# Kernel optimization log

Measured on AMD Instinct MI355X. Metric: run time of the kernel, lower is better.

The kernel has to match this reference:

```python
import jax, jax.numpy as jnp
import numpy as np

HIDDEN = 2048
NUM_HEADS = 16
NUM_KV_HEADS = 4
HEAD_DIM = 128
ROPE_BASE = 10000.0


def apply_rope(x):
    # x: [B, H, S, D]; standard half-split RoPE
    B, H, S, D = x.shape
    half = D // 2
    inv_freq = 1.0 / (ROPE_BASE ** (jnp.arange(half, dtype=jnp.float32) / half))
    ang = jnp.arange(S, dtype=jnp.float32)[:, None] * inv_freq[None, :]  # [S, half]
    cos = jnp.cos(ang).astype(x.dtype)
    sin = jnp.sin(ang).astype(x.dtype)
    x1, x2 = x[..., :half], x[..., half:]
    return jnp.concatenate([x1 * cos - x2 * sin, x1 * sin + x2 * cos], axis=-1)


def setup_inputs() -> dict:
    key = jax.random.key(0)
    ks = jax.random.split(key, 6)
    B, S = 2, 2048
    sd = 1.0 / np.sqrt(HIDDEN)
    x = jax.random.normal(ks[0], (B, S, HIDDEN), dtype=jnp.float32)
    wq = jax.random.normal(ks[1], (NUM_HEADS * HEAD_DIM, HIDDEN), dtype=jnp.float32) * sd
    wk = jax.random.normal(ks[2], (NUM_KV_HEADS * HEAD_DIM, HIDDEN), dtype=jnp.float32) * sd
    wv = jax.random.normal(ks[3], (NUM_KV_HEADS * HEAD_DIM, HIDDEN), dtype=jnp.float32) * sd
    wo = jax.random.normal(ks[4], (HIDDEN, NUM_HEADS * HEAD_DIM), dtype=jnp.float32) * sd
    key_weights = jnp.ones((NUM_HEADS,), dtype=jnp.float32)
    return {"x": x, "wq": wq, "wk": wk, "wv": wv, "wo": wo, "key_weights": key_weights}


def reference(x, wq, wk, wv, wo, key_weights):
    B, S, _ = x.shape
    g = NUM_HEADS // NUM_KV_HEADS
    scale = HEAD_DIM ** -0.5
    # projections -> [B, H, S, D]
    q = (x @ wq.T).reshape(B, S, NUM_HEADS, HEAD_DIM).transpose(0, 2, 1, 3)
    k = (x @ wk.T).reshape(B, S, NUM_KV_HEADS, HEAD_DIM).transpose(0, 2, 1, 3)
    v = (x @ wv.T).reshape(B, S, NUM_KV_HEADS, HEAD_DIM).transpose(0, 2, 1, 3)
    q = apply_rope(q)
    k = apply_rope(k)
    # GQA expansion (repeat_interleave over head dim)
    k = jnp.repeat(k, g, axis=1)
    v = jnp.repeat(v, g, axis=1)
    # per-head key scaling fused into K
    k = k * key_weights[None, :, None, None]
    scores = jnp.einsum("bhqd,bhkd->bhqk", q, k) * scale
    causal = jnp.triu(jnp.ones((S, S), dtype=bool), k=1)
    scores = jnp.where(causal, -jnp.inf, scores)
    attn = jax.nn.softmax(scores, axis=-1)
    out = jnp.einsum("bhqk,bhkd->bhqd", attn, v)
    out = out.transpose(0, 2, 1, 3).reshape(B, S, NUM_HEADS * HEAD_DIM)
    return out @ wo.T
```

## Files before the change

kernel.cpp:

```cpp
#include <hip/hip_runtime.h>

#define S_LEN 2048
#define HID 2048
#define NH 16
#define HD 128
#define QKV_N 3072
#define KCOL 2048
#define VCOL 2560

typedef unsigned short ushort_t;
using bf16x8 = __attribute__((ext_vector_type(8))) __bf16;
using f32x4 = __attribute__((ext_vector_type(4))) float;
using ushort8 = __attribute__((ext_vector_type(8))) unsigned short;
using ushort4v = __attribute__((ext_vector_type(4))) unsigned short;

__device__ __forceinline__ unsigned short f2bf(float f) {
  unsigned int u = __float_as_uint(f);
  unsigned int r = u + 0x7FFFu + ((u >> 16) & 1u);
  return (unsigned short)(r >> 16);
}
__device__ __forceinline__ float bf2f(unsigned short h) {
  return __uint_as_float(((unsigned int)h) << 16);
}

__device__ __forceinline__ void gload_lds16(const ushort_t* g, ushort_t* lds) {
  __builtin_amdgcn_global_load_lds(
      (const __attribute__((address_space(1))) unsigned int*)g,
      (__attribute__((address_space(3))) unsigned int*)lds, 16, 0, 0);
}

__global__ void cast_bf16_kernel(const float* __restrict__ in, ushort_t* __restrict__ out, int n4) {
  int i = blockIdx.x * 256 + threadIdx.x;
  if (i >= n4) return;
  float4 v = reinterpret_cast<const float4*>(in)[i];
  ushort4v o;
  o.x = f2bf(v.x); o.y = f2bf(v.y); o.z = f2bf(v.z); o.w = f2bf(v.w);
  reinterpret_cast<ushort4v*>(out)[i] = o;
}

__global__ void rope_table_kernel(float* __restrict__ cosT, float* __restrict__ sinT) {
  int i = blockIdx.x * 256 + threadIdx.x;
  if (i >= S_LEN * 64) return;
  int s = i >> 6, j = i & 63;
  float inv = __expf(-(float)j * (9.210340371976184f / 64.0f));
  float ang = (float)s * inv;
  float sv, cv;
  sincosf(ang, &sv, &cv);
  cosT[i] = cv;
  sinT[i] = sv;
}

__global__ void rope_apply_kernel(ushort_t* __restrict__ base, const float* __restrict__ cosT,
                                  const float* __restrict__ sinT, const float* __restrict__ kw,
                                  int stride, int lognh, float scale, int useKw, int n) {
  int idx = blockIdx.x * 256 + threadIdx.x;
  if (idx >= n) return;
  int row = idx >> lognh;
  int p = idx & ((1 << lognh) - 1);
  int h = p >> 6, j = p & 63;
  int s = row & (S_LEN - 1);
  float c = cosT[(s << 6) + j];
  float sn = sinT[(s << 6) + j];
  long a = (long)row * stride + h * HD;
  float x1 = bf2f(base[a + j]);
  float x2 = bf2f(base[a + j + 64]);
  float wsc = useKw ? (scale * kw[h]) : scale;
  base[a + j] = f2bf((x1 * c - x2 * sn) * wsc);
  base[a + j + 64] = f2bf((x1 * sn + x2 * c) * wsc);
}

__global__ __launch_bounds__(256) void transpose_v_kernel(const ushort_t* __restrict__ qkv,
                                                          ushort_t* __restrict__ vt) {
  __shared__ ushort_t T[64][76];
  int bid = blockIdx.x;
  int dd = bid & 7;
  int tt = bid >> 3;
  int tid = threadIdx.x;
#pragma unroll
  for (int it = 0; it < 2; ++it) {
    int c = tid + it * 256;
    int i = c >> 3, j8 = c & 7;
    ushort8 v = *reinterpret_cast<const ushort8*>(
        qkv + (long)(tt * 64 + i) * QKV_N + VCOL + dd * 64 + j8 * 8);
    *reinterpret_cast<ushort8*>(&T[i][j8 * 8]) = v;
  }
  __syncthreads();
#pragma unroll
  for (int it = 0; it < 2; ++it) {
    int c = tid + it * 256;
    int jd = c >> 3, sc = c & 7;
    ushort8 o;
#pragma unroll
    for (int e = 0; e < 8; ++e) o[e] = T[sc * 8 + e][jd];
    int token = tt * 64 + sc * 8;
    int b = token >> 11, s = token & (S_LEN - 1);
    int vd = dd * 64 + jd;
    *reinterpret_cast<ushort8*>(vt + ((long)(b * 512 + vd) << 11) + s) = o;
  }
}

__device__ __forceinline__ void store_c(ushort_t* p, float v) { *p = f2bf(v); }
__device__ __forceinline__ void store_c(float* p, float v) { *p = v; }

template <typename OT>
__global__ __launch_bounds__(256) void gemm_bt_kernel(const ushort_t* __restrict__ A,
                                                      const ushort_t* __restrict__ W,
                                                      OT* __restrict__ C, int M, int N, int K) {
  __shared__ ushort_t As[128 * 32];
  __shared__ ushort_t Bs[128 * 32];
  const int tid = threadIdx.x;
  const int l = tid & 63, w = tid >> 6;
  const int wr = w >> 1, wc = w & 1;
  const int r = l & 15, g = l >> 4;
  const long arow0 = (long)blockIdx.y * 128;
  const long brow0 = (long)blockIdx.x * 128;

  f32x4 acc[4][4] = {};

  const int c0 = tid, c1 = tid + 256;
  const ushort_t* a_src0 = A + (arow0 + (c0 >> 2)) * K + ((c0 & 3) << 3);
  const ushort_t* a_src1 = A + (arow0 + (c1 >> 2)) * K + ((c1 & 3) << 3);
  const ushort_t* b_src0 = W + (brow0 + (c0 >> 2)) * K + ((c0 & 3) << 3);
  const ushort_t* b_src1 = W + (brow0 + (c1 >> 2)) * K + ((c1 & 3) << 3);
  ushort_t* a_dst0 = &As[c0 * 8];
  ushort_t* a_dst1 = &As[c1 * 8];
  ushort_t* b_dst0 = &Bs[c0 * 8];
  ushort_t* b_dst1 = &Bs[c1 * 8];

  for (int kk = 0; kk < K; kk += 32) {
    gload_lds16(a_src0 + kk, a_dst0);
    gload_lds16(a_src1 + kk, a_dst1);
    gload_lds16(b_src0 + kk, b_dst0);
    gload_lds16(b_src1 + kk, b_dst1);
    __syncthreads();
    bf16x8 af[4], bw[4];
#pragma unroll
    for (int mi = 0; mi < 4; ++mi)
      af[mi] = *reinterpret_cast<const bf16x8*>(&As[(wr * 64 + mi * 16 + r) * 32 + g * 8]);
#pragma unroll
    for (int ni = 0; ni < 4; ++ni)
      bw[ni] = *reinterpret_cast<const bf16x8*>(&Bs[(wc * 64 + ni * 16 + r) * 32 + g * 8]);
#pragma unroll
    for (int mi = 0; mi < 4; ++mi)
#pragma unroll
      for (int ni = 0; ni < 4; ++ni)
        acc[mi][ni] = __builtin_amdgcn_mfma_f32_16x16x32_bf16(af[mi], bw[ni], acc[mi][ni], 0, 0, 0);
    __syncthreads();
  }

#pragma unroll
  for (int mi = 0; mi < 4; ++mi)
#pragma unroll
    for (int ni = 0; ni < 4; ++ni) {
      int col = (int)brow0 + wc * 64 + ni * 16 + r;
#pragma unroll
      for (int j = 0; j < 4; ++j) {
        int row = (int)arow0 + wr * 64 + mi * 16 + g * 4 + j;
        store_c(&C[(long)row * N + col], acc[mi][ni][j]);
      }
    }
}

__device__ __forceinline__ void stage_tile(const ushort_t* __restrict__ Kb,
                                           const ushort_t* __restrict__ Vb, int kv,
                                           ushort_t* __restrict__ KsBuf,
                                           ushort_t* __restrict__ VtsBuf, int tid) {
#pragma unroll
  for (int i = 0; i < 4; ++i) {
    int c = tid + i * 256;
    int krow = c >> 4, cc = c & 15;
    int scc = cc ^ (krow & 7);
    gload_lds16(Kb + (long)(kv * 64 + krow) * QKV_N + scc * 8, &KsBuf[c * 8]);
  }
#pragma unroll
  for (int i = 0; i < 4; ++i) {
    int c = tid + i * 256;
    int vrow = c >> 3, cc = c & 7;
    int scc = cc ^ (vrow & 7);
    gload_lds16(Vb + ((long)vrow << 11) + kv * 64 + scc * 8, &VtsBuf[c * 8]);
  }
}

__global__ __launch_bounds__(256) void flash_attn_kernel(const ushort_t* __restrict__ qkv,
                                                         const ushort_t* __restrict__ Vt,
                                                         ushort_t* __restrict__ AO) {
  __shared__ ushort_t Ks[2][64 * 128];
  __shared__ ushort_t Vts[2][128 * 64];
  __shared__ ushort_t Ps[4][16 * 64];

  const int d = blockIdx.x;
  const int o = (d & 7) * 64 + (d >> 3);
  const int pr = o & 15;
  const int h = (o >> 4) & 15;
  const int b = o >> 8;
  const int tid = threadIdx.x;
  const int l = tid & 63, w = tid >> 6;
  const int r = l & 15, g = l >> 4;
  const int kvh = h >> 2;

  const ushort_t* Qb = qkv + (long)b * S_LEN * QKV_N + h * HD;
  const ushort_t* Kb = qkv + (long)b * S_LEN * QKV_N + KCOL + kvh * HD;
  const ushort_t* Vb = Vt + ((long)(b * 512 + kvh * HD) << 11);

  for (int pi = 0; pi < 2; ++pi) {
    const int qt = pi ? (31 - pr) : pr;
    const int qg = qt * 64 + w * 16;
    const long qrow0 = (long)b * S_LEN + qg;

    bf16x8 qa[4];
#pragma unroll
    for (int ks = 0; ks < 4; ++ks)
      qa[ks] = *reinterpret_cast<const bf16x8*>(Qb + (long)(qg + r) * QKV_N + ks * 32 + g * 8);

    f32x4 acc[8] = {};
    float mrow[4], lrow[4];
#pragma unroll
    for (int j = 0; j < 4; ++j) { mrow[j] = -1e30f; lrow[j] = 0.f; }

    stage_tile(Kb, Vb, 0, Ks[0], Vts[0], tid);
    __syncthreads();
    int cur = 0;

    for (int kv = 0; kv <= qt; ++kv) {
      if (kv < qt) stage_tile(Kb, Vb, kv + 1, Ks[cur ^ 1], Vts[cur ^ 1], tid);
      const ushort_t* KsC = Ks[cur];
      const ushort_t* VtsC = Vts[cur];

      f32x4 s[4] = {};
#pragma unroll
      for (int ks = 0; ks < 4; ++ks) {
        bf16x8 kf[4];
#pragma unroll
        for (int ni = 0; ni < 4; ++ni) {
          int n = ni * 16 + r;
          int chunk = (ks * 4 + g) ^ (n & 7);
          kf[ni] = *reinterpret_cast<const bf16x8*>(
              reinterpret_cast<const char*>(KsC) + n * 256 + chunk * 16);
        }
#pragma unroll
        for (int ni = 0; ni < 4; ++ni)
          s[ni] = __builtin_amdgcn_mfma_f32_16x16x32_bf16(qa[ks], kf[ni], s[ni], 0, 0, 0);
      }
      if (kv == qt) {
#pragma unroll
        for (int ni = 0; ni < 4; ++ni) {
          int key = kv * 64 + ni * 16 + r;
#pragma unroll
          for (int j = 0; j < 4; ++j) {
            int rowq = qg + g * 4 + j;
            if (key > rowq) s[ni][j] = -1e30f;
          }
        }
      }
#pragma unroll
      for (int j = 0; j < 4; ++j) {
        float mx = fmaxf(fmaxf(s[0][j], s[1][j]), fmaxf(s[2][j], s[3][j]));
        mx = fmaxf(mx, __shfl_xor(mx, 1));
        mx = fmaxf(mx, __shfl_xor(mx, 2));
        mx = fmaxf(mx, __shfl_xor(mx, 4));
        mx = fmaxf(mx, __shfl_xor(mx, 8));
        float mo = mrow[j];
        float mn = fmaxf(mo, mx);
        float ef = __expf(mo - mn);
        mrow[j] = mn;
        float psum = 0.f;
#pragma unroll
        for (int ni = 0; ni < 4; ++ni) {
          float p = __expf(s[ni][j] - mn);
          s[ni][j] = p;
          psum += p;
        }
        lrow[j] = lrow[j] * ef + psum;
#pragma unroll
        for (int ni = 0; ni < 8; ++ni) acc[ni][j] *= ef;
      }
#pragma unroll
      for (int ni = 0; ni < 4; ++ni)
#pragma unroll
        for (int j = 0; j < 4; ++j) {
          int row = g * 4 + j;
          int chunk = (ni * 2 + (r >> 3)) ^ (row & 7);
          Ps[w][row * 64 + chunk * 8 + (r & 7)] = f2bf(s[ni][j]);
        }
#pragma unroll
      for (int ks2 = 0; ks2 < 2; ++ks2) {
        bf16x8 pa = *reinterpret_cast<const bf16x8*>(
            &Ps[w][r * 64 + (((ks2 * 4 + g) ^ (r & 7)) << 3)]);
#pragma unroll
        for (int ni = 0; ni < 8; ++ni) {
          int dd = ni * 16 + r;
          int chunk = (ks2 * 4 + g) ^ (dd & 7);
          bf16x8 vf = *reinterpret_cast<const bf16x8*>(
              reinterpret_cast<const char*>(VtsC) + dd * 128 + chunk * 16);
          acc[ni] = __builtin_amdgcn_mfma_f32_16x16x32_bf16(pa, vf, acc[ni], 0, 0, 0);
        }
      }
      __syncthreads();
      cur ^= 1;
    }

#pragma unroll
    for (int j = 0; j < 4; ++j) {
      float lt = lrow[j];
      lt += __shfl_xor(lt, 1);
      lt += __shfl_xor(lt, 2);
      lt += __shfl_xor(lt, 4);
      lt += __shfl_xor(lt, 8);
      float inv = 1.0f / lt;
#pragma unroll
      for (int ni = 0; ni < 8; ++ni) acc[ni][j] *= inv;
    }
#pragma unroll
    for (int ni = 0; ni < 8; ++ni) {
      int col = h * HD + ni * 16 + r;
#pragma unroll
      for (int j = 0; j < 4; ++j) {
        long row = qrow0 + g * 4 + j;
        AO[row * HID + col] = f2bf(acc[ni][j]);
      }
    }
  }
}

extern "C" void kernel_launch(void* const* d_in, const int* in_sizes, int n_in,
                              void* d_out, int out_size, void* d_ws, size_t ws_size,
                              hipStream_t stream) {
  const float* x = (const float*)d_in[0];
  const float* wq = (const float*)d_in[1];
  const float* wk = (const float*)d_in[2];
  const float* wv = (const float*)d_in[3];
  const float* wo = (const float*)d_in[4];
  const float* kw = (const float*)d_in[5];
  float* out = (float*)d_out;

  ushort_t* ws = (ushort_t*)d_ws;
  ushort_t* xb = ws;
  ushort_t* qkv = xb + 8388608;
  ushort_t* vt = qkv + 12582912;
  ushort_t* wqkv = vt + 2097152;
  float* cosT = (float*)(wqkv + 6291456);
  float* sinT = cosT + S_LEN * 64;

  cast_bf16_kernel<<<8192, 256, 0, stream>>>(x, xb, 2097152);
  cast_bf16_kernel<<<4096, 256, 0, stream>>>(wq, wqkv, 1048576);
  cast_bf16_kernel<<<1024, 256, 0, stream>>>(wk, wqkv + 2048 * 2048, 262144);
  cast_bf16_kernel<<<1024, 256, 0, stream>>>(wv, wqkv + 2560 * 2048, 262144);
  rope_table_kernel<<<512, 256, 0, stream>>>(cosT, sinT);

  gemm_bt_kernel<ushort_t><<<dim3(24, 32), 256, 0, stream>>>(xb, wqkv, qkv, 4096, QKV_N, 2048);

  rope_apply_kernel<<<16384, 256, 0, stream>>>(qkv, cosT, sinT, kw, QKV_N, 10,
                                               0.08838834764831845f, 1, 4194304);
  rope_apply_kernel<<<4096, 256, 0, stream>>>(qkv + KCOL, cosT, sinT, kw, QKV_N, 8,
                                              1.0f, 0, 1048576);

  transpose_v_kernel<<<512, 256, 0, stream>>>(qkv, vt);

  ushort_t* wob = wqkv;
  cast_bf16_kernel<<<4096, 256, 0, stream>>>(wo, wob, 1048576);

  flash_attn_kernel<<<512, 256, 0, stream>>>(qkv, vt, xb);

  gemm_bt_kernel<float><<<dim3(16, 32), 256, 0, stream>>>(xb, wob, out, 4096, 2048, 2048);
}
```

Baseline: 352.8 us.

## Fuse cast and RoPE launches, add 256x256 double-buffered QKV GEMM

```diff
diff --git a/kernel.cpp b/kernel.cpp
--- a/kernel.cpp
+++ b/kernel.cpp
@@ -29,6 +29,23 @@
       (__attribute__((address_space(3))) unsigned int*)lds, 16, 0, 0);
 }
 
+__global__ void cast_fused_kernel(const float* __restrict__ x, const float* __restrict__ wq,
+                                  const float* __restrict__ wk, const float* __restrict__ wv,
+                                  ushort_t* __restrict__ xb, ushort_t* __restrict__ wqkv) {
+  int i = blockIdx.x * 256 + threadIdx.x;
+  const float* src;
+  ushort_t* dst;
+  int li;
+  if (i < 2097152) { src = x; dst = xb; li = i; }
+  else if (i < 3145728) { src = wq; dst = wqkv; li = i - 2097152; }
+  else if (i < 3407872) { src = wk; dst = wqkv + 4194304; li = i - 3145728; }
+  else { src = wv; dst = wqkv + 5242880; li = i - 3407872; }
+  float4 v = reinterpret_cast<const float4*>(src)[li];
+  ushort4v o;
+  o.x = f2bf(v.x); o.y = f2bf(v.y); o.z = f2bf(v.z); o.w = f2bf(v.w);
+  reinterpret_cast<ushort4v*>(dst)[li] = o;
+}
+
 __global__ void cast_bf16_kernel(const float* __restrict__ in, ushort_t* __restrict__ out, int n4) {
   int i = blockIdx.x * 256 + threadIdx.x;
   if (i >= n4) return;
@@ -38,35 +55,44 @@
   reinterpret_cast<ushort4v*>(out)[i] = o;
 }
 
-__global__ void rope_table_kernel(float* __restrict__ cosT, float* __restrict__ sinT) {
-  int i = blockIdx.x * 256 + threadIdx.x;
-  if (i >= S_LEN * 64) return;
-  int s = i >> 6, j = i & 63;
-  float inv = __expf(-(float)j * (9.210340371976184f / 64.0f));
-  float ang = (float)s * inv;
-  float sv, cv;
-  sincosf(ang, &sv, &cv);
-  cosT[i] = cv;
-  sinT[i] = sv;
-}
-
-__global__ void rope_apply_kernel(ushort_t* __restrict__ base, const float* __restrict__ cosT,
-                                  const float* __restrict__ sinT, const float* __restrict__ kw,
-                                  int stride, int lognh, float scale, int useKw, int n) {
+__global__ void rope_fused_kernel(ushort_t* __restrict__ qkv, const float* __restrict__ kw) {
   int idx = blockIdx.x * 256 + threadIdx.x;
-  if (idx >= n) return;
-  int row = idx >> lognh;
-  int p = idx & ((1 << lognh) - 1);
-  int h = p >> 6, j = p & 63;
+  int row, colbase, j0;
+  float wsc;
+  if (idx < 524288) {
+    row = idx >> 7;
+    int p = idx & 127;
+    int h = p >> 3;
+    j0 = (p & 7) * 8;
+    colbase = h * HD;
+    wsc = 0.08838834764831845f * kw[h];
+  } else {
+    int t = idx - 524288;
+    row = t >> 5;
+    int p = t & 31;
+    int h = p >> 3;
+    j0 = (p & 7) * 8;
+    colbase = KCOL + h * HD;
+    wsc = 1.0f;
+  }
   int s = row & (S_LEN - 1);
-  float c = cosT[(s << 6) + j];
-  float sn = sinT[(s << 6) + j];
-  long a = (long)row * stride + h * HD;
-  float x1 = bf2f(base[a + j]);
-  float x2 = bf2f(base[a + j + 64]);
-  float wsc = useKw ? (scale * kw[h]) : scale;
-  base[a + j] = f2bf((x1 * c - x2 * sn) * wsc);
-  base[a + j + 64] = f2bf((x1 * sn + x2 * c) * wsc);
+  long base = (long)row * QKV_N + colbase;
+  ushort8 x1 = *reinterpret_cast<const ushort8*>(qkv + base + j0);
+  ushort8 x2 = *reinterpret_cast<const ushort8*>(qkv + base + j0 + 64);
+  ushort8 o1, o2;
+#pragma unroll
+  for (int e = 0; e < 8; ++e) {
+    int j = j0 + e;
+    float inv = __expf(-(float)j * (9.210340371976184f / 64.0f));
+    float ang = (float)s * inv;
+    float sv, cv;
+    sincosf(ang, &sv, &cv);
+    float a = bf2f(x1[e]), bb = bf2f(x2[e]);
+    o1[e] = f2bf((a * cv - bb * sv) * wsc);
+    o2[e] = f2bf((a * sv + bb * cv) * wsc);
+  }
+  *reinterpret_cast<ushort8*>(qkv + base + j0) = o1;
+  *reinterpret_cast<ushort8*>(qkv + base + j0 + 64) = o2;
 }
 
 __global__ __launch_bounds__(256) void transpose_v_kernel(const ushort_t* __restrict__ qkv,
@@ -161,6 +187,111 @@
     }
 }
 
+__device__ __forceinline__ void stage256(const ushort_t* __restrict__ Ag,
+                                         const ushort_t* __restrict__ Wg, int kk, int K,
+                                         ushort_t* __restrict__ AsB, ushort_t* __restrict__ BsB,
+                                         int tid) {
+#pragma unroll
+  for (int i = 0; i < 4; ++i) {
+    int c = tid + i * 512;
+    int row = c >> 3, cc = c & 7;
+    int scc = cc ^ (row & 7);
+    gload_lds16(Ag + (long)row * K + kk + scc * 8, &AsB[c * 8]);
+  }
+#pragma unroll
+  for (int i = 0; i < 4; ++i) {
+    int c = tid + i * 512;
+    int row = c >> 3, cc = c & 7;
+    int scc = cc ^ (row & 7);
+    gload_lds16(Wg + (long)row * K + kk + scc * 8, &BsB[c * 8]);
+  }
+}
+
+__global__ __launch_bounds__(512, 2) void gemm256_kernel(const ushort_t* __restrict__ A,
+                                                         const ushort_t* __restrict__ W,
+                                                         ushort_t* __restrict__ C, int M, int N,
+                                                         int K, int nbx) {
+  __shared__ ushort_t As[2][256 * 64];
+  __shared__ ushort_t Bs[2][256 * 64];
+
+  const int nwg = (M >> 8) * nbx;
+  const int cpx = nwg >> 3;
+  const int o = (blockIdx.x & 7) * cpx + (blockIdx.x >> 3);
+  const int bx = o % nbx, by = o / nbx;
+
+  const int tid = threadIdx.x;
+  const int l = tid & 63, w = tid >> 6;
+  const int wr = w >> 2, wc = w & 3;
+  const int r = l & 15, g = l >> 4;
+  const long arow0 = (long)by * 256;
+  const long bcol0 = (long)bx * 256;
+  const ushort_t* Ag = A + arow0 * K;
+  const ushort_t* Wg = W + bcol0 * K;
+
+  f32x4 acc[8][4] = {};
+
+  stage256(Ag, Wg, 0, K, As[0], Bs[0], tid);
+  __syncthreads();
+  int cur = 0;
+  const int nt = K >> 6;
+
+  for (int kt = 0; kt < nt; ++kt) {
+    if (kt + 1 < nt) stage256(Ag, Wg, (kt + 1) << 6, K, As[cur ^ 1], Bs[cur ^ 1], tid);
+    const ushort_t* AsC = As[cur];
+    const ushort_t* BsC = Bs[cur];
+
+    bf16x8 bw[4][2];
+#pragma unroll
+    for (int ni = 0; ni < 4; ++ni)
+#pragma unroll
+      for (int ks = 0; ks < 2; ++ks) {
+        int row = wc * 64 + ni * 16 + r;
+        int chunk = (ks * 4 + g) ^ (r & 7);
+        bw[ni][ks] = *reinterpret_cast<const bf16x8*>(&BsC[row * 64 + chunk * 8]);
+      }
+#pragma unroll
+    for (int ph = 0; ph < 4; ++ph) {
+      bf16x8 af[2][2];
+#pragma unroll
+      for (int m2 = 0; m2 < 2; ++m2)
+#pragma unroll
+        for (int ks = 0; ks < 2; ++ks) {
+          int row = wr * 128 + (ph * 2 + m2) * 16 + r;
+          int chunk = (ks * 4 + g) ^ (r & 7);
+          af[m2][ks] = *reinterpret_cast<const bf16x8*>(&AsC[row * 64 + chunk * 8]);
+        }
+      __builtin_amdgcn_s_barrier();
+      asm volatile("s_waitcnt lgkmcnt(0)" ::: "memory");
+      __builtin_amdgcn_sched_barrier(0);
+      __builtin_amdgcn_s_setprio(1);
+#pragma unroll
+      for (int m2 = 0; m2 < 2; ++m2)
+#pragma unroll
+        for (int ni = 0; ni < 4; ++ni)
+#pragma unroll
+          for (int ks = 0; ks < 2; ++ks)
+            acc[ph * 2 + m2][ni] =
+                __builtin_amdgcn_mfma_f32_16x16x32_bf16(af[m2][ks], bw[ni][ks],
+                                                        acc[ph * 2 + m2][ni], 0, 0, 0);
+      __builtin_amdgcn_s_setprio(0);
+    }
+    __syncthreads();
+    cur ^= 1;
+  }
+
+#pragma unroll
+  for (int mi = 0; mi < 8; ++mi)
+#pragma unroll
+    for (int ni = 0; ni < 4; ++ni) {
+      long col = bcol0 + wc * 64 + ni * 16 + r;
+#pragma unroll
+      for (int j = 0; j < 4; ++j) {
+        long row = arow0 + wr * 128 + mi * 16 + g * 4 + j;
+        C[row * N + col] = f2bf(acc[mi][ni][j]);
+      }
+    }
+}
+
 __device__ __forceinline__ void stage_tile(const ushort_t* __restrict__ Kb,
                                            const ushort_t* __restrict__ Vb, int kv,
                                            ushort_t* __restrict__ KsBuf,
@@ -338,21 +469,12 @@
   ushort_t* qkv = xb + 8388608;
   ushort_t* vt = qkv + 12582912;
   ushort_t* wqkv = vt + 2097152;
-  float* cosT = (float*)(wqkv + 6291456);
-  float* sinT = cosT + S_LEN * 64;
-
-  cast_bf16_kernel<<<8192, 256, 0, stream>>>(x, xb, 2097152);
-  cast_bf16_kernel<<<4096, 256, 0, stream>>>(wq, wqkv, 1048576);
-  cast_bf16_kernel<<<1024, 256, 0, stream>>>(wk, wqkv + 2048 * 2048, 262144);
-  cast_bf16_kernel<<<1024, 256, 0, stream>>>(wv, wqkv + 2560 * 2048, 262144);
-  rope_table_kernel<<<512, 256, 0, stream>>>(cosT, sinT);
-
-  gemm_bt_kernel<ushort_t><<<dim3(24, 32), 256, 0, stream>>>(xb, wqkv, qkv, 4096, QKV_N, 2048);
-
-  rope_apply_kernel<<<16384, 256, 0, stream>>>(qkv, cosT, sinT, kw, QKV_N, 10,
-                                               0.08838834764831845f, 1, 4194304);
-  rope_apply_kernel<<<4096, 256, 0, stream>>>(qkv + KCOL, cosT, sinT, kw, QKV_N, 8,
-                                              1.0f, 0, 1048576);
+
+  cast_fused_kernel<<<14336, 256, 0, stream>>>(x, wq, wk, wv, xb, wqkv);
+
+  gemm256_kernel<<<192, 512, 0, stream>>>(xb, wqkv, qkv, 4096, QKV_N, 2048, 12);
+
+  rope_fused_kernel<<<2560, 256, 0, stream>>>(qkv, kw);
 
   transpose_v_kernel<<<512, 256, 0, stream>>>(qkv, vt);
 
```

After: 342.0 us. 1.03x faster.
